# Kernel tuning notes

Measured on AMD Instinct MI355X. Metric: run time of the kernel, lower is better.

The kernel has to match this reference:

```python
import jax, jax.numpy as jnp
import numpy as np

MASK_THR = 0.2
EPS = 1e-12  # torch F.normalize eps


def setup_inputs() -> dict:
    key = jax.random.key(0)
    k1, k2, k3 = jax.random.split(key, 3)
    B, Cin, H, W = 2, 384, 96, 96
    features = jax.random.normal(k1, (B, Cin, H, W), dtype=jnp.float32)
    # projector: Conv2d(384,256,1) -> ReLU -> Conv2d(256,128,1); 1x1 convs == per-pixel GEMMs
    W1 = jax.random.normal(k2, (256, Cin), dtype=jnp.float32) * (1.0 / np.sqrt(Cin))
    b1 = jnp.zeros((256,), dtype=jnp.float32)
    W2 = jax.random.normal(k3, (128, 256), dtype=jnp.float32) * (1.0 / np.sqrt(256))
    b2 = jnp.zeros((128,), dtype=jnp.float32)
    return {"features": features, "W1": W1, "b1": b1, "W2": W2, "b2": b2}


def reference(features, W1, b1, W2, b2):
    B, _, H, Wd = features.shape
    # projector (1x1 convs as channel GEMMs)
    h = jax.nn.relu(jnp.einsum('oc,bchw->bohw', W1, features) + b1[None, :, None, None])
    feat = jnp.einsum('oc,bchw->bohw', W2, h) + b2[None, :, None, None]  # [B,128,H,W]
    # get_mask: L2-normalize over channels, full pairwise similarity, top-2 NN, distance, threshold
    norm = jnp.sqrt(jnp.sum(feat * feat, axis=1, keepdims=True))
    nf = feat / jnp.maximum(norm, EPS)
    C = nf.shape[1]
    rf = jnp.transpose(nf, (0, 2, 3, 1)).reshape(B, H * Wd, C)         # [B,N,C]
    sim = jnp.einsum('bnc,bmc->bnm', rf, rf)                           # [B,N,N]
    _, top2_idx = jax.lax.top_k(sim, 2)
    nn_idx = top2_idx[:, :, 1]                                         # nearest non-self neighbor
    nearest = jnp.take_along_axis(rf, nn_idx[:, :, None], axis=1)      # [B,N,C]
    diff = rf - nearest
    distance = jnp.sqrt(jnp.sum(diff * diff, axis=-1))                 # [B,N]
    mask = (distance > MASK_THR).astype(feat.dtype).reshape(B, 1, H, Wd)
    return mask, distance
```

## Files before the change

kernel.cpp:

```cpp
#include <hip/hip_runtime.h>

#define NHW 9216
#define NB 2
#define NCHUNK 16

typedef short s8v __attribute__((ext_vector_type(8)));
typedef _Float16 h8v __attribute__((ext_vector_type(8)));
typedef float f4v __attribute__((ext_vector_type(4)));
typedef unsigned int u32;
typedef unsigned short u16;

__device__ inline u16 f2bf(float x) {
    u32 u = __float_as_uint(x);
    u += 0x7fffu + ((u >> 16) & 1u);
    return (u16)(u >> 16);
}
__device__ inline u16 f2h(float x) {
    _Float16 h = (_Float16)x;
    return *(u16*)&h;
}

__global__ __launch_bounds__(256) void k_xsplit(const float* __restrict__ X,
                                                u16* __restrict__ xh)
{
    __shared__ float fs[64][65];
    const int tid = threadIdx.x;
    const int b = blockIdx.z, p0 = blockIdx.x * 64, half = blockIdx.y;
    const size_t fb = (size_t)b * 384 * NHW;
    const int px = tid >> 2, sub = tid & 3;
    const size_t g = (size_t)b * NHW + p0 + px;
    for (int pass = half * 3; pass < half * 3 + 3; ++pass) {
        int c0p = pass * 64;
        __syncthreads();
#pragma unroll
        for (int r = 0; r < 16; ++r) {
            int e = r * 256 + tid;
            int cc = e >> 6, p = e & 63;
            fs[cc][p] = X[fb + (size_t)(c0p + cc) * NHW + p0 + p];
        }
        __syncthreads();
        u16 hb[16];
#pragma unroll
        for (int i = 0; i < 16; ++i) hb[i] = f2h(fs[sub * 16 + i][px]);
        size_t o = g * 384 + c0p + sub * 16;
        *(s8v*)&xh[o]     = *(s8v*)&hb[0];
        *(s8v*)&xh[o + 8] = *(s8v*)&hb[8];
    }
}

__global__ __launch_bounds__(256) void k_wsplit(const float* __restrict__ W1,
                                                const float* __restrict__ W2,
                                                u16* __restrict__ w1h, u16* __restrict__ w1l,
                                                u16* __restrict__ w2h, u16* __restrict__ w2l)
{
    int i = blockIdx.x * 256 + threadIdx.x;
    if (i < 98304) {
        float v = W1[i];
        _Float16 h = (_Float16)v;
        w1h[i] = *(u16*)&h;
        w1l[i] = f2h(v - (float)h);
    } else {
        int j = i - 98304;
        float v = W2[j];
        _Float16 h = (_Float16)v;
        w2h[j] = *(u16*)&h;
        w2l[j] = f2h(v - (float)h);
    }
}

__global__ __launch_bounds__(256, 4) void k_gemm1(const u16* __restrict__ xh,
                                                  const u16* __restrict__ w1h, const u16* __restrict__ w1l,
                                                  const float* __restrict__ b1,
                                                  u16* __restrict__ hh)
{
    union __align__(16) SM {
        struct { u16 B[2][16][512]; } stg;
        u16 bounce[128 * 66];
    };
    __shared__ SM sm;
    const int tid = threadIdx.x;
    const int wave = tid >> 6, l = tid & 63, l15 = l & 15, q = l >> 4;
    const int bx = blockIdx.x;
    const int xcd = bx & 7, k = bx >> 3;
    const int g0 = (xcd * 18 + (k >> 2)) * 128;
    const int c0 = (k & 3) * 64;
    const int gw = g0 + wave * 32;

    auto stage = [&](int kt, int buf) {
#pragma unroll
        for (int r = 0; r < 4; ++r) {
            int cid = r * 4 + wave;
            int spl = cid >> 3, kf = (cid >> 2) & 1, cs = cid & 3;
            const u16* src = (spl ? w1l : w1h) + (size_t)(c0 + cs * 16 + l15) * 384 + kt + kf * 32 + q * 8;
            __builtin_amdgcn_global_load_lds(
                (const __attribute__((address_space(1))) void*)src,
                (__attribute__((address_space(3))) void*)&sm.stg.B[buf][cid][0],
                16, 0, 0);
        }
    };

    f4v acc[2][4];
#pragma unroll
    for (int s = 0; s < 2; ++s)
#pragma unroll
        for (int c = 0; c < 4; ++c) acc[s][c] = (f4v){0.f, 0.f, 0.f, 0.f};

    stage(0, 0);
    __syncthreads();
    for (int t = 0; t < 6; ++t) {
        const int kt = t * 64;
        const int buf = t & 1;
        if (t < 5) stage(kt + 64, buf ^ 1);
        s8v ah[2][2];
#pragma unroll
        for (int s = 0; s < 2; ++s)
#pragma unroll
            for (int kf = 0; kf < 2; ++kf)
                ah[s][kf] = *(const s8v*)&xh[(size_t)(gw + s * 16 + l15) * 384 + kt + kf * 32 + q * 8];
#pragma unroll
        for (int kf = 0; kf < 2; ++kf)
#pragma unroll
            for (int cs = 0; cs < 4; ++cs) {
                s8v bh = *(const s8v*)&sm.stg.B[buf][kf * 4 + cs][l * 8];
                s8v bl = *(const s8v*)&sm.stg.B[buf][8 + kf * 4 + cs][l * 8];
#pragma unroll
                for (int s = 0; s < 2; ++s) {
                    acc[s][cs] = __builtin_amdgcn_mfma_f32_16x16x32_f16(*(h8v*)&ah[s][kf], *(h8v*)&bh, acc[s][cs], 0, 0, 0);
                    acc[s][cs] = __builtin_amdgcn_mfma_f32_16x16x32_f16(*(h8v*)&ah[s][kf], *(h8v*)&bl, acc[s][cs], 0, 0, 0);
                }
            }
        __syncthreads();
    }

#pragma unroll
    for (int s = 0; s < 2; ++s)
#pragma unroll
        for (int cs = 0; cs < 4; ++cs) {
            int c = cs * 16 + l15;
            float bv = b1[c0 + c];
#pragma unroll
            for (int r = 0; r < 4; ++r) {
                int px = wave * 32 + s * 16 + q * 4 + r;
                sm.bounce[px * 66 + c] = f2h(fmaxf(acc[s][cs][r] + bv, 0.f));
            }
        }
    __syncthreads();
    {
        int px = tid >> 1, half = tid & 1;
        u32 tmp[16];
#pragma unroll
        for (int j = 0; j < 16; ++j)
            tmp[j] = *(const u32*)&sm.bounce[px * 66 + half * 32 + j * 2];
        size_t o = (size_t)(g0 + px) * 256 + c0 + half * 32;
#pragma unroll
        for (int j = 0; j < 4; ++j)
            *(s8v*)&hh[o + j * 8] = ((s8v*)tmp)[j];
    }
}

__global__ __launch_bounds__(256, 4) void k_gemm2(const u16* __restrict__ hh,
                                                  const u16* __restrict__ w2h, const u16* __restrict__ w2l,
                                                  const float* __restrict__ b2,
                                                  float* __restrict__ feat)
{
    __shared__ u16 Bs[32][512];
    const int tid = threadIdx.x;
    const int wave = tid >> 6, l = tid & 63, l15 = l & 15, q = l >> 4;
    const int bx = blockIdx.x;
    const int xcd = bx & 7, k = bx >> 3;
    const int g0 = (xcd * 18 + (k >> 2)) * 128;
    const int c0 = (k & 3) * 32;

#pragma unroll
    for (int r = 0; r < 8; ++r) {
        int cid = r * 4 + wave;
        int spl = cid >> 4, kf = (cid >> 1) & 7, cs = cid & 1;
        const u16* src = (spl ? w2l : w2h) + (size_t)(c0 + cs * 16 + l15) * 256 + kf * 32 + q * 8;
        __builtin_amdgcn_global_load_lds(
            (const __attribute__((address_space(1))) void*)src,
            (__attribute__((address_space(3))) void*)&Bs[cid][0],
            16, 0, 0);
    }
    __syncthreads();

    const int gw = g0 + wave * 32;
    f4v acc[2][2];
#pragma unroll
    for (int s = 0; s < 2; ++s)
#pragma unroll
        for (int c = 0; c < 2; ++c) acc[s][c] = (f4v){0.f, 0.f, 0.f, 0.f};

#pragma unroll
    for (int kf = 0; kf < 8; ++kf) {
        s8v ah[2];
#pragma unroll
        for (int s = 0; s < 2; ++s)
            ah[s] = *(const s8v*)&hh[(size_t)(gw + s * 16 + l15) * 256 + kf * 32 + q * 8];
#pragma unroll
        for (int cs = 0; cs < 2; ++cs) {
            s8v bh = *(const s8v*)&Bs[kf * 2 + cs][l * 8];
            s8v bl = *(const s8v*)&Bs[16 + kf * 2 + cs][l * 8];
#pragma unroll
            for (int s = 0; s < 2; ++s) {
                acc[s][cs] = __builtin_amdgcn_mfma_f32_16x16x32_f16(*(h8v*)&ah[s], *(h8v*)&bh, acc[s][cs], 0, 0, 0);
                acc[s][cs] = __builtin_amdgcn_mfma_f32_16x16x32_f16(*(h8v*)&ah[s], *(h8v*)&bl, acc[s][cs], 0, 0, 0);
            }
        }
    }
#pragma unroll
    for (int s = 0; s < 2; ++s)
#pragma unroll
        for (int cs = 0; cs < 2; ++cs) {
            float bv = b2[c0 + cs * 16 + l15];
#pragma unroll
            for (int r = 0; r < 4; ++r)
                feat[(size_t)(gw + s * 16 + q * 4 + r) * 128 + c0 + cs * 16 + l15] = acc[s][cs][r] + bv;
        }
}

__global__ __launch_bounds__(256) void k_norm2(const float* __restrict__ feat,
                                               float* __restrict__ rf,
                                               u16* __restrict__ hib)
{
    const int tid = threadIdx.x;
    const int px = blockIdx.x * 32 + (tid >> 3), part = tid & 7;
    const size_t o = (size_t)px * 128 + part * 16;
    f4v v[4];
    float ss = 0.f;
#pragma unroll
    for (int j = 0; j < 4; ++j) {
        v[j] = *(const f4v*)&feat[o + j * 4];
        ss += v[j][0]*v[j][0] + v[j][1]*v[j][1] + v[j][2]*v[j][2] + v[j][3]*v[j][3];
    }
    ss += __shfl_xor(ss, 1, 64);
    ss += __shfl_xor(ss, 2, 64);
    ss += __shfl_xor(ss, 4, 64);
    const float mx = fmaxf(sqrtf(ss), 1e-12f);
    u16 hb[16];
#pragma unroll
    for (int j = 0; j < 4; ++j) {
        f4v w;
#pragma unroll
        for (int e = 0; e < 4; ++e) {
            float val = v[j][e] / mx;
            w[e] = val;
            hb[j * 4 + e] = f2bf(val);
        }
        *(f4v*)&rf[o + j * 4] = w;
    }
    *(s8v*)&hib[o]     = *(s8v*)&hb[0];
    *(s8v*)&hib[o + 8] = *(s8v*)&hb[8];
}

__global__ __launch_bounds__(256, 2) void k_simtop(const u16* __restrict__ hi,
                                                   int* __restrict__ cidx)
{
    __shared__ u16 Bs[2][16][512];
    const int tid  = threadIdx.x;
    const int wave = tid >> 6, l = tid & 63, l15 = l & 15, q = l >> 4;
    const int b     = blockIdx.z;
    const int rbase = blockIdx.x * 256;
    const int chunk = blockIdx.y;
    const int cbase = chunk * 576;
    const size_t base = (size_t)b * NHW;
    const int wr0 = rbase + wave * 64;

    s8v ah[4][4];
#pragma unroll
    for (int s = 0; s < 4; ++s) {
        int row = wr0 + s * 16 + l15;
#pragma unroll
        for (int kf = 0; kf < 4; ++kf)
            ah[s][kf] = *(const s8v*)&hi[(base + row) * 128 + kf * 32 + q * 8];
    }

    auto stage = [&](int colt, int buf) {
#pragma unroll
        for (int r = 0; r < 4; ++r) {
            int cid = r * 4 + wave;
            int kf = cid >> 2, cs = cid & 3;
            int col = colt + cs * 16 + l15;
            const u16* src = hi + (base + col) * 128 + kf * 32 + q * 8;
            __builtin_amdgcn_global_load_lds(
                (const __attribute__((address_space(1))) void*)src,
                (__attribute__((address_space(3))) void*)&Bs[buf][cid][0],
                16, 0, 0);
        }
    };

    u32 bk[4][4];
#pragma unroll
    for (int s = 0; s < 4; ++s)
#pragma unroll
        for (int r = 0; r < 4; ++r) bk[s][r] = 0u;

    stage(cbase, 0);
    __syncthreads();

    for (int ct = 0; ct < 9; ++ct) {
        const int colt = cbase + ct * 64;
        const int buf  = ct & 1;
        if (ct < 8) stage(colt + 64, buf ^ 1);

        f4v acc[4][4];
#pragma unroll
        for (int s = 0; s < 4; ++s)
#pragma unroll
            for (int c = 0; c < 4; ++c) acc[s][c] = (f4v){2.f, 2.f, 2.f, 2.f};

#pragma unroll
        for (int kf = 0; kf < 4; ++kf)
#pragma unroll
            for (int cs = 0; cs < 4; ++cs) {
                s8v bh = *(const s8v*)&Bs[buf][kf * 4 + cs][l * 8];
#pragma unroll
                for (int s = 0; s < 4; ++s)
                    acc[s][cs] = __builtin_amdgcn_mfma_f32_16x16x32_bf16(ah[s][kf], bh, acc[s][cs], 0, 0, 0);
            }

        const u32 tagv = (u32)(ct << 2);
        const bool hasdiag = (colt < wr0 + 64) && (wr0 < colt + 64);
        if (hasdiag) {
#pragma unroll
            for (int s = 0; s < 4; ++s)
#pragma unroll
                for (int r = 0; r < 4; ++r) {
                    const int rr = wr0 + s * 16 + q * 4 + r;
                    u32 km = 0u;
#pragma unroll
                    for (int cs = 0; cs < 4; ++cs) {
                        u32 kk = (__float_as_uint(acc[s][cs][r]) & 0xffffffc0u) | (tagv | (u32)cs);
                        if (colt + cs * 16 + l15 == rr) kk = 0u;
                        km = kk > km ? kk : km;
                    }
                    bk[s][r] = km > bk[s][r] ? km : bk[s][r];
                }
        } else {
#pragma unroll
            for (int s = 0; s < 4; ++s)
#pragma unroll
                for (int r = 0; r < 4; ++r) {
                    u32 km = 0u;
#pragma unroll
                    for (int cs = 0; cs < 4; ++cs) {
                        u32 kk = (__float_as_uint(acc[s][cs][r]) & 0xffffffc0u) | (tagv | (u32)cs);
                        km = kk > km ? kk : km;
                    }
                    bk[s][r] = km > bk[s][r] ? km : bk[s][r];
                }
        }
        __syncthreads();
    }

#pragma unroll
    for (int s = 0; s < 4; ++s)
#pragma unroll
        for (int r = 0; r < 4; ++r) {
            u32 key = bk[s][r];
            float v = __uint_as_float(key & 0xffffffc0u);
            int ctw = (int)((key >> 2) & 15u);
            int csw = (int)(key & 3u);
            int col = cbase + ctw * 64 + csw * 16 + l15;
#pragma unroll
            for (int d = 1; d < 16; d <<= 1) {
                float ov = __shfl_xor(v, d, 64);
                int   oi = __shfl_xor(col, d, 64);
                bool p = (ov > v) || (ov == v && oi < col);
                v   = p ? ov : v;
                col = p ? oi : col;
            }
            if (l15 == 0) {
                int row = wr0 + s * 16 + q * 4 + r;
                cidx[(base + row) * NCHUNK + chunk] = col;
            }
        }
}

__global__ __launch_bounds__(256) void k_finish(const float* __restrict__ rf,
                                                const int* __restrict__ cidx,
                                                float* __restrict__ out)
{
    const int tid = threadIdx.x;
    const int g = blockIdx.x * 16 + (tid >> 4);
    const int l15 = tid & 15;
    const int b = g / NHW;
    const size_t rowbase = (size_t)b * NHW;

    const float* x = rf + (size_t)g * 128;
    f4v x0 = *(const f4v*)&x[l15 * 8];
    f4v x1 = *(const f4v*)&x[l15 * 8 + 4];

    float bestS = -2.f; int bestI = 0;
#pragma unroll
    for (int j = 0; j < NCHUNK; ++j) {
        int c = cidx[(size_t)g * NCHUNK + j];
        const float* y = rf + (rowbase + c) * 128;
        f4v y0 = *(const f4v*)&y[l15 * 8];
        f4v y1 = *(const f4v*)&y[l15 * 8 + 4];
        float s = x0[0]*y0[0] + x0[1]*y0[1] + x0[2]*y0[2] + x0[3]*y0[3]
                + x1[0]*y1[0] + x1[1]*y1[1] + x1[2]*y1[2] + x1[3]*y1[3];
#pragma unroll
        for (int d = 1; d < 16; d <<= 1) s += __shfl_xor(s, d, 64);
        bool p = (s > bestS) || (s == bestS && c < bestI);
        bestS = p ? s : bestS;
        bestI = p ? c : bestI;
    }

    const float* y = rf + (rowbase + bestI) * 128;
    f4v y0 = *(const f4v*)&y[l15 * 8];
    f4v y1 = *(const f4v*)&y[l15 * 8 + 4];
    float d0 = x0[0]-y0[0], d1 = x0[1]-y0[1], d2 = x0[2]-y0[2], d3 = x0[3]-y0[3];
    float e0 = x1[0]-y1[0], e1 = x1[1]-y1[1], e2 = x1[2]-y1[2], e3 = x1[3]-y1[3];
    float ss = d0*d0 + d1*d1 + d2*d2 + d3*d3 + e0*e0 + e1*e1 + e2*e2 + e3*e3;
#pragma unroll
    for (int d = 1; d < 16; d <<= 1) ss += __shfl_xor(ss, d, 64);
    if (l15 == 0) {
        float dist = sqrtf(ss);
        out[NB * NHW + g] = dist;
        out[g] = dist > 0.2f ? 1.0f : 0.0f;
    }
}

extern "C" void kernel_launch(void* const* d_in, const int* in_sizes, int n_in,
                              void* d_out, int out_size, void* d_ws, size_t ws_size,
                              hipStream_t stream) {
    const float* features = (const float*)d_in[0];
    const float* W1 = (const float*)d_in[1];
    const float* b1 = (const float*)d_in[2];
    const float* W2 = (const float*)d_in[3];
    const float* b2 = (const float*)d_in[4];
    float* out = (float*)d_out;
    float* ws  = (float*)d_ws;

    u16*   xh   = (u16*)ws;
    u16*   hh   = (u16*)(ws + 3538944);
    u16*   w1h  = (u16*)(ws + 5898240);
    u16*   w1l  = (u16*)(ws + 5947392);
    u16*   w2h  = (u16*)(ws + 5996544);
    u16*   w2l  = (u16*)(ws + 6012928);
    float* feat = ws;
    u16*   hib  = (u16*)(ws + 2359296);
    float* rf   = ws + 3538944;
    int*   cidx = (int*)ws;

    k_xsplit<<<dim3(144, 2, NB), 256, 0, stream>>>(features, xh);
    k_wsplit<<<512, 256, 0, stream>>>(W1, W2, w1h, w1l, w2h, w2l);
    k_gemm1<<<576, 256, 0, stream>>>(xh, w1h, w1l, b1, hh);
    k_gemm2<<<576, 256, 0, stream>>>(hh, w2h, w2l, b2, feat);
    k_norm2<<<576, 256, 0, stream>>>(feat, rf, hib);
    k_simtop<<<dim3(36, NCHUNK, NB), 256, 0, stream>>>(hib, cidx);
    k_finish<<<1152, 256, 0, stream>>>(rf, cidx, out);
}
```

Measured before the change: 202.5 us.

## Fuse normalization into GEMM2, drop W2 low-split, retile simtop for occupancy

GEMM2 now computes all 128 output channels per block, so the per-pixel L2 normalization and the bf16 conversion happen in registers. This removes the separate norm kernel and the fp32 feat round trip through memory. The W2 fp16 hi/lo split is dropped, halving the GEMM2 MFMA work at some cost in precision of the projected features. The similarity/top-k kernel is retiled to 192 rows per block (48 per wave) with occupancy 3 to spread more blocks across CUs.

```diff
diff --git a/kernel.cpp b/kernel.cpp
--- a/kernel.cpp
+++ b/kernel.cpp
@@ -51,7 +51,7 @@
 __global__ __launch_bounds__(256) void k_wsplit(const float* __restrict__ W1,
                                                 const float* __restrict__ W2,
                                                 u16* __restrict__ w1h, u16* __restrict__ w1l,
-                                                u16* __restrict__ w2h, u16* __restrict__ w2l)
+                                                u16* __restrict__ w2h)
 {
     int i = blockIdx.x * 256 + threadIdx.x;
     if (i < 98304) {
@@ -61,10 +61,7 @@
         w1l[i] = f2h(v - (float)h);
     } else {
         int j = i - 98304;
-        float v = W2[j];
-        _Float16 h = (_Float16)v;
-        w2h[j] = *(u16*)&h;
-        w2l[j] = f2h(v - (float)h);
+        w2h[j] = f2h(W2[j]);
     }
 }
 
@@ -158,24 +155,24 @@
     }
 }
 
-__global__ __launch_bounds__(256, 4) void k_gemm2(const u16* __restrict__ hh,
-                                                  const u16* __restrict__ w2h, const u16* __restrict__ w2l,
-                                                  const float* __restrict__ b2,
-                                                  float* __restrict__ feat)
-{
-    __shared__ u16 Bs[32][512];
+__global__ __launch_bounds__(256) void k_gemm2n(const u16* __restrict__ hh,
+                                                const u16* __restrict__ w2h,
+                                                const float* __restrict__ b2,
+                                                float* __restrict__ rf,
+                                                u16* __restrict__ hib)
+{
+    __shared__ u16 Bs[64][512];
     const int tid = threadIdx.x;
     const int wave = tid >> 6, l = tid & 63, l15 = l & 15, q = l >> 4;
     const int bx = blockIdx.x;
     const int xcd = bx & 7, k = bx >> 3;
-    const int g0 = (xcd * 18 + (k >> 2)) * 128;
-    const int c0 = (k & 3) * 32;
-
-#pragma unroll
-    for (int r = 0; r < 8; ++r) {
+    const int g0 = (xcd * 36 + k) * 64;
+
+#pragma unroll
+    for (int r = 0; r < 16; ++r) {
         int cid = r * 4 + wave;
-        int spl = cid >> 4, kf = (cid >> 1) & 7, cs = cid & 1;
-        const u16* src = (spl ? w2l : w2h) + (size_t)(c0 + cs * 16 + l15) * 256 + kf * 32 + q * 8;
+        int kf = cid >> 3, cst = cid & 7;
+        const u16* src = w2h + (size_t)(cst * 16 + l15) * 256 + kf * 32 + q * 8;
         __builtin_amdgcn_global_load_lds(
             (const __attribute__((address_space(1))) void*)src,
             (__attribute__((address_space(3))) void*)&Bs[cid][0],
@@ -183,91 +180,66 @@
     }
     __syncthreads();
 
-    const int gw = g0 + wave * 32;
-    f4v acc[2][2];
-#pragma unroll
-    for (int s = 0; s < 2; ++s)
-#pragma unroll
-        for (int c = 0; c < 2; ++c) acc[s][c] = (f4v){0.f, 0.f, 0.f, 0.f};
+    const int gw = g0 + wave * 16;
+    f4v acc[8];
+#pragma unroll
+    for (int c = 0; c < 8; ++c) acc[c] = (f4v){0.f, 0.f, 0.f, 0.f};
 
 #pragma unroll
     for (int kf = 0; kf < 8; ++kf) {
-        s8v ah[2];
-#pragma unroll
-        for (int s = 0; s < 2; ++s)
-            ah[s] = *(const s8v*)&hh[(size_t)(gw + s * 16 + l15) * 256 + kf * 32 + q * 8];
-#pragma unroll
-        for (int cs = 0; cs < 2; ++cs) {
-            s8v bh = *(const s8v*)&Bs[kf * 2 + cs][l * 8];
-            s8v bl = *(const s8v*)&Bs[16 + kf * 2 + cs][l * 8];
-#pragma unroll
-            for (int s = 0; s < 2; ++s) {
-                acc[s][cs] = __builtin_amdgcn_mfma_f32_16x16x32_f16(*(h8v*)&ah[s], *(h8v*)&bh, acc[s][cs], 0, 0, 0);
-                acc[s][cs] = __builtin_amdgcn_mfma_f32_16x16x32_f16(*(h8v*)&ah[s], *(h8v*)&bl, acc[s][cs], 0, 0, 0);
-            }
-        }
-    }
-#pragma unroll
-    for (int s = 0; s < 2; ++s)
-#pragma unroll
-        for (int cs = 0; cs < 2; ++cs) {
-            float bv = b2[c0 + cs * 16 + l15];
-#pragma unroll
-            for (int r = 0; r < 4; ++r)
-                feat[(size_t)(gw + s * 16 + q * 4 + r) * 128 + c0 + cs * 16 + l15] = acc[s][cs][r] + bv;
-        }
-}
-
-__global__ __launch_bounds__(256) void k_norm2(const float* __restrict__ feat,
-                                               float* __restrict__ rf,
-                                               u16* __restrict__ hib)
-{
-    const int tid = threadIdx.x;
-    const int px = blockIdx.x * 32 + (tid >> 3), part = tid & 7;
-    const size_t o = (size_t)px * 128 + part * 16;
-    f4v v[4];
-    float ss = 0.f;
-#pragma unroll
-    for (int j = 0; j < 4; ++j) {
-        v[j] = *(const f4v*)&feat[o + j * 4];
-        ss += v[j][0]*v[j][0] + v[j][1]*v[j][1] + v[j][2]*v[j][2] + v[j][3]*v[j][3];
-    }
-    ss += __shfl_xor(ss, 1, 64);
-    ss += __shfl_xor(ss, 2, 64);
-    ss += __shfl_xor(ss, 4, 64);
-    const float mx = fmaxf(sqrtf(ss), 1e-12f);
-    u16 hb[16];
-#pragma unroll
-    for (int j = 0; j < 4; ++j) {
-        f4v w;
-#pragma unroll
-        for (int e = 0; e < 4; ++e) {
-            float val = v[j][e] / mx;
-            w[e] = val;
-            hb[j * 4 + e] = f2bf(val);
-        }
-        *(f4v*)&rf[o + j * 4] = w;
-    }
-    *(s8v*)&hib[o]     = *(s8v*)&hb[0];
-    *(s8v*)&hib[o + 8] = *(s8v*)&hb[8];
-}
-
-__global__ __launch_bounds__(256, 2) void k_simtop(const u16* __restrict__ hi,
+        s8v ah = *(const s8v*)&hh[(size_t)(gw + l15) * 256 + kf * 32 + q * 8];
+#pragma unroll
+        for (int cst = 0; cst < 8; ++cst) {
+            s8v bh = *(const s8v*)&Bs[kf * 8 + cst][l * 8];
+            acc[cst] = __builtin_amdgcn_mfma_f32_16x16x32_f16(*(h8v*)&ah, *(h8v*)&bh, acc[cst], 0, 0, 0);
+        }
+    }
+
+    float ssq[4] = {0.f, 0.f, 0.f, 0.f};
+#pragma unroll
+    for (int cst = 0; cst < 8; ++cst) {
+        float bv = b2[cst * 16 + l15];
+#pragma unroll
+        for (int r = 0; r < 4; ++r) {
+            acc[cst][r] += bv;
+            ssq[r] += acc[cst][r] * acc[cst][r];
+        }
+    }
+#pragma unroll
+    for (int r = 0; r < 4; ++r) {
+        ssq[r] += __shfl_xor(ssq[r], 1, 64);
+        ssq[r] += __shfl_xor(ssq[r], 2, 64);
+        ssq[r] += __shfl_xor(ssq[r], 4, 64);
+        ssq[r] += __shfl_xor(ssq[r], 8, 64);
+        ssq[r] = 1.0f / fmaxf(sqrtf(ssq[r]), 1e-12f);
+    }
+#pragma unroll
+    for (int cst = 0; cst < 8; ++cst)
+#pragma unroll
+        for (int r = 0; r < 4; ++r) {
+            float val = acc[cst][r] * ssq[r];
+            size_t o = (size_t)(gw + q * 4 + r) * 128 + cst * 16 + l15;
+            rf[o]  = val;
+            hib[o] = f2bf(val);
+        }
+}
+
+__global__ __launch_bounds__(256, 3) void k_simtop(const u16* __restrict__ hi,
                                                    int* __restrict__ cidx)
 {
     __shared__ u16 Bs[2][16][512];
     const int tid  = threadIdx.x;
     const int wave = tid >> 6, l = tid & 63, l15 = l & 15, q = l >> 4;
     const int b     = blockIdx.z;
-    const int rbase = blockIdx.x * 256;
+    const int rbase = blockIdx.x * 192;
     const int chunk = blockIdx.y;
     const int cbase = chunk * 576;
     const size_t base = (size_t)b * NHW;
-    const int wr0 = rbase + wave * 64;
-
-    s8v ah[4][4];
-#pragma unroll
-    for (int s = 0; s < 4; ++s) {
+    const int wr0 = rbase + wave * 48;
+
+    s8v ah[3][4];
+#pragma unroll
+    for (int s = 0; s < 3; ++s) {
         int row = wr0 + s * 16 + l15;
 #pragma unroll
         for (int kf = 0; kf < 4; ++kf)
@@ -288,9 +260,9 @@
         }
     };
 
-    u32 bk[4][4];
-#pragma unroll
-    for (int s = 0; s < 4; ++s)
+    u32 bk[3][4];
+#pragma unroll
+    for (int s = 0; s < 3; ++s)
 #pragma unroll
         for (int r = 0; r < 4; ++r) bk[s][r] = 0u;
 
@@ -302,9 +274,9 @@
         const int buf  = ct & 1;
         if (ct < 8) stage(colt + 64, buf ^ 1);
 
-        f4v acc[4][4];
-#pragma unroll
-        for (int s = 0; s < 4; ++s)
+        f4v acc[3][4];
+#pragma unroll
+        for (int s = 0; s < 3; ++s)
 #pragma unroll
             for (int c = 0; c < 4; ++c) acc[s][c] = (f4v){2.f, 2.f, 2.f, 2.f};
 
@@ -314,15 +286,15 @@
             for (int cs = 0; cs < 4; ++cs) {
                 s8v bh = *(const s8v*)&Bs[buf][kf * 4 + cs][l * 8];
 #pragma unroll
-                for (int s = 0; s < 4; ++s)
+                for (int s = 0; s < 3; ++s)
                     acc[s][cs] = __builtin_amdgcn_mfma_f32_16x16x32_bf16(ah[s][kf], bh, acc[s][cs], 0, 0, 0);
             }
 
         const u32 tagv = (u32)(ct << 2);
-        const bool hasdiag = (colt < wr0 + 64) && (wr0 < colt + 64);
+        const bool hasdiag = (colt < wr0 + 48) && (wr0 < colt + 64);
         if (hasdiag) {
 #pragma unroll
-            for (int s = 0; s < 4; ++s)
+            for (int s = 0; s < 3; ++s)
 #pragma unroll
                 for (int r = 0; r < 4; ++r) {
                     const int rr = wr0 + s * 16 + q * 4 + r;
@@ -337,7 +309,7 @@
                 }
         } else {
 #pragma unroll
-            for (int s = 0; s < 4; ++s)
+            for (int s = 0; s < 3; ++s)
 #pragma unroll
                 for (int r = 0; r < 4; ++r) {
                     u32 km = 0u;
@@ -353,7 +325,7 @@
     }
 
 #pragma unroll
-    for (int s = 0; s < 4; ++s)
+    for (int s = 0; s < 3; ++s)
 #pragma unroll
         for (int r = 0; r < 4; ++r) {
             u32 key = bk[s][r];
@@ -437,17 +409,14 @@
     u16*   w1h  = (u16*)(ws + 5898240);
     u16*   w1l  = (u16*)(ws + 5947392);
     u16*   w2h  = (u16*)(ws + 5996544);
-    u16*   w2l  = (u16*)(ws + 6012928);
-    float* feat = ws;
+    float* rf   = ws;
     u16*   hib  = (u16*)(ws + 2359296);
-    float* rf   = ws + 3538944;
-    int*   cidx = (int*)ws;
+    int*   cidx = (int*)(ws + 3538944);
 
     k_xsplit<<<dim3(144, 2, NB), 256, 0, stream>>>(features, xh);
-    k_wsplit<<<512, 256, 0, stream>>>(W1, W2, w1h, w1l, w2h, w2l);
+    k_wsplit<<<512, 256, 0, stream>>>(W1, W2, w1h, w1l, w2h);
     k_gemm1<<<576, 256, 0, stream>>>(xh, w1h, w1l, b1, hh);
-    k_gemm2<<<576, 256, 0, stream>>>(hh, w2h, w2l, b2, feat);
-    k_norm2<<<576, 256, 0, stream>>>(feat, rf, hib);
-    k_simtop<<<dim3(36, NCHUNK, NB), 256, 0, stream>>>(hib, cidx);
+    k_gemm2n<<<288, 256, 0, stream>>>(hh, w2h, b2, rf, hib);
+    k_simtop<<<dim3(48, NCHUNK, NB), 256, 0, stream>>>(hib, cidx);
     k_finish<<<1152, 256, 0, stream>>>(rf, cidx, out);
 }
```

New measurement: 187.0 us. 1.08x faster.
